# Kernel tuning notes

Hardware: AMD Instinct MI355X
Metric: run time of the kernel (lower is better)

The kernel has to match this reference:

```python
import jax, jax.numpy as jnp
import numpy as np

EPS = 1e-5  # PyTorch BatchNorm3d default eps

def _bn(x, gamma, beta, mean, var):
    # eval-mode batchnorm over channel dim (axis=1) of [B,C,D,H,W]
    inv = jax.lax.rsqrt(var + EPS)
    scale = (gamma * inv)[None, :, None, None, None]
    shift = (beta - mean * gamma * inv)[None, :, None, None, None]
    return x * scale + shift

def _pconv(x, w):
    # 1x1x1 conv3d == channel contraction: w [O,C], x [B,C,D,H,W]
    return jnp.einsum('oc,bcdhw->bodhw', w, x)

def setup_inputs() -> dict:
    key = jax.random.key(0)
    ks = jax.random.split(key, 12)
    B, G, D, H, W = 4, 8, 48, 128, 160
    x1 = jax.random.normal(ks[0], (B, G, D, H, W), dtype=jnp.float32)
    # conv0: G->16 (no bias), BN params for 16 channels
    w0 = jax.random.normal(ks[1], (16, G), dtype=jnp.float32) * 0.1
    g0 = jnp.ones((16,), jnp.float32)
    b0 = jnp.zeros((16,), jnp.float32)
    m0 = jax.random.normal(ks[2], (16,), dtype=jnp.float32) * 0.01
    v0 = jax.random.uniform(ks[3], (16,), jnp.float32, 0.5, 1.5)
    # conv1: 16->8 (no bias), BN params for 8 channels
    w1 = jax.random.normal(ks[4], (8, 16), dtype=jnp.float32) * 0.1
    g1 = jnp.ones((8,), jnp.float32)
    b1 = jnp.zeros((8,), jnp.float32)
    m1 = jax.random.normal(ks[5], (8,), dtype=jnp.float32) * 0.01
    v1 = jax.random.uniform(ks[6], (8,), jnp.float32, 0.5, 1.5)
    # conv2: 8->1 with bias (xavier init)
    lim = float(np.sqrt(6.0 / (8 + 1)))
    w2 = jax.random.uniform(ks[7], (1, 8), jnp.float32, -lim, lim)
    b2 = jnp.zeros((1,), jnp.float32)
    return {"x1": x1, "w0": w0, "g0": g0, "b0": b0, "m0": m0, "v0": v0,
            "w1": w1, "g1": g1, "b1": b1, "m1": m1, "v1": v1,
            "w2": w2, "b2": b2}

def reference(x1, w0, g0, b0, m0, v0, w1, g1, b1, m1, v1, w2, b2):
    h = jax.nn.relu(_bn(_pconv(x1, w0), g0, b0, m0, v0))   # [B,16,D,H,W]
    h = jax.nn.relu(_bn(_pconv(h, w1), g1, b1, m1, v1))    # [B,8,D,H,W]
    h = _pconv(h, w2) + b2[None, :, None, None, None]      # [B,1,D,H,W]
    h = jnp.squeeze(h, axis=1)                             # view -> [B,D,H,W]
    out = jnp.max(jax.nn.sigmoid(h), axis=1)               # max over depth
    return out[:, None]                                    # [B,1,H,W]
```

## Files before the change

### kernel.cpp

```cpp
#include <hip/hip_runtime.h>

#define BATCH 4
#define CIN   8
#define DEPTH 48
#define HGT   128
#define WID   160

#define HW    (HGT*WID)
#define DHW   (DEPTH*HW)
#define CDHW  (CIN*DHW)
#define NPIX  (BATCH*HW)

#define DSPLIT 8
#define DCHUNK (DEPTH/DSPLIT)
#define TILES_PER_B (HW/128)
#define NTILES (NPIX/128)

#define WS_W0P 0
#define WS_S0F 64
#define WS_W1P 80
#define WS_S1F 144
#define WS_W2F 152
#define WS_B2F 160
#define WS_FLAG 384
#define WS_PART 512

typedef _Float16 half2_t __attribute__((ext_vector_type(2)));

static __device__ __forceinline__ float asf(unsigned int u) {
    return __builtin_bit_cast(float, u);
}
static __device__ __forceinline__ unsigned int asu(float f) {
    return __builtin_bit_cast(unsigned int, f);
}
static __device__ __forceinline__ unsigned int pkrtz_u(float a, float b) {
    return __builtin_bit_cast(unsigned int, __builtin_amdgcn_cvt_pkrtz(a, b));
}
static __device__ __forceinline__ float fdot2_u(unsigned int a, unsigned int b, float c) {
    return __builtin_amdgcn_fdot2(__builtin_bit_cast(half2_t, a),
                                  __builtin_bit_cast(half2_t, b), c, false);
}
static __device__ __forceinline__ float ldp(const void* p, int i, bool bf) {
    if (bf) {
        unsigned int u = ((const unsigned short*)p)[i];
        return asf(u << 16);
    }
    return ((const float*)p)[i];
}

__global__ void prep_kernel(const unsigned int* __restrict__ x,
                            const void* __restrict__ w0, const void* __restrict__ g0,
                            const void* __restrict__ b0, const void* __restrict__ m0,
                            const void* __restrict__ v0, const void* __restrict__ w1,
                            const void* __restrict__ g1, const void* __restrict__ b1,
                            const void* __restrict__ m1, const void* __restrict__ v1,
                            const void* __restrict__ w2, const void* __restrict__ b2,
                            float* __restrict__ ws)
{
    unsigned int* wsu = (unsigned int*)ws;
    int t = threadIdx.x;

    int cnt = 0;
    #pragma unroll
    for (int i = 0; i < 16; ++i) {
        unsigned int v = x[(unsigned)(t * 997 + i * 61440 + 12345)];
        if ((((v >> 8) & 0x78u)) == 0x38u) ++cnt;
    }
    #pragma unroll
    for (int off = 32; off > 0; off >>= 1) cnt += __shfl_down(cnt, off, 64);
    cnt = __shfl(cnt, 0, 64);
    bool bf = (cnt >= 512);
    if (t == 0) wsu[WS_FLAG] = bf ? 1u : 0u;

    if (t < 16) {
        float sc = ldp(g0, t, bf) * rsqrtf(ldp(v0, t, bf) + 1e-5f);
        for (int c = 0; c < 4; ++c)
            wsu[WS_W0P + t*4 + c] = pkrtz_u(ldp(w0, t*8 + 2*c, bf) * sc,
                                            ldp(w0, t*8 + 2*c + 1, bf) * sc);
        ws[WS_S0F + t] = ldp(b0, t, bf) - ldp(m0, t, bf) * sc;
    }
    if (t < 8) {
        float sc = ldp(g1, t, bf) * rsqrtf(ldp(v1, t, bf) + 1e-5f);
        for (int c = 0; c < 8; ++c)
            wsu[WS_W1P + t*8 + c] = pkrtz_u(ldp(w1, t*16 + 2*c, bf) * sc,
                                            ldp(w1, t*16 + 2*c + 1, bf) * sc);
        ws[WS_S1F + t] = ldp(b1, t, bf) - ldp(m1, t, bf) * sc;
        ws[WS_W2F + t] = ldp(w2, t, bf);
    }
    if (t == 0) ws[WS_B2F] = ldp(b2, 0, bf);
}

__global__ __launch_bounds__(64, 2) void main_kernel(const void* __restrict__ xv,
                                                     const float* __restrict__ ws,
                                                     float* __restrict__ part)
{
    const unsigned int* wsu = (const unsigned int*)ws;
    bool bf = (wsu[WS_FLAG] != 0u);
    const unsigned int* xb = (const unsigned int*)xv;
    const float2*      xf = (const float2*)xv;

    int lane = threadIdx.x;
    int bid  = blockIdx.x;
    int tile = bid % NTILES;
    int dc   = bid / NTILES;
    int b    = tile / TILES_PER_B;
    int hwp  = (tile % TILES_PER_B) * 64 + lane;
    unsigned bbase = (unsigned)(b * (CDHW/2)) + (unsigned)hwp;
    int d0 = dc * DCHUNK;

    unsigned int W0p[64], W1p[64];
    float S0[16], S1[8], W2[8];
    {
        const uint4* q0 = (const uint4*)(wsu + WS_W0P);
        #pragma unroll
        for (int i = 0; i < 16; ++i) { uint4 q = q0[i]; W0p[4*i]=q.x; W0p[4*i+1]=q.y; W0p[4*i+2]=q.z; W0p[4*i+3]=q.w; }
        const uint4* q1 = (const uint4*)(wsu + WS_W1P);
        #pragma unroll
        for (int i = 0; i < 16; ++i) { uint4 q = q1[i]; W1p[4*i]=q.x; W1p[4*i+1]=q.y; W1p[4*i+2]=q.z; W1p[4*i+3]=q.w; }
        const float4* qs = (const float4*)(ws + WS_S0F);
        #pragma unroll
        for (int i = 0; i < 4; ++i) { float4 f = qs[i]; S0[4*i]=f.x; S0[4*i+1]=f.y; S0[4*i+2]=f.z; S0[4*i+3]=f.w; }
        const float4* qt = (const float4*)(ws + WS_S1F);
        #pragma unroll
        for (int i = 0; i < 2; ++i) { float4 f = qt[i]; S1[4*i]=f.x; S1[4*i+1]=f.y; S1[4*i+2]=f.z; S1[4*i+3]=f.w; }
        const float4* qw = (const float4*)(ws + WS_W2F);
        #pragma unroll
        for (int i = 0; i < 2; ++i) { float4 f = qw[i]; W2[4*i]=f.x; W2[4*i+1]=f.y; W2[4*i+2]=f.z; W2[4*i+3]=f.w; }
    }
    float B2v = ws[WS_B2F];

    float mA = -1e30f, mB = -1e30f;

    #pragma unroll 2
    for (int dd = 0; dd < DCHUNK; ++dd) {
        int d = d0 + dd;
        unsigned idx0 = bbase + (unsigned)(d * (HW/2));

        unsigned int xA[4], xB[4];
        if (bf) {
            unsigned int xd[8];
            #pragma unroll
            for (int c = 0; c < 8; ++c) xd[c] = xb[idx0 + (unsigned)(c * (DHW/2))];
            #pragma unroll
            for (int j = 0; j < 4; ++j) {
                xA[j] = pkrtz_u(asf(xd[2*j] << 16),        asf(xd[2*j+1] << 16));
                xB[j] = pkrtz_u(asf(xd[2*j] & 0xFFFF0000u), asf(xd[2*j+1] & 0xFFFF0000u));
            }
        } else {
            float2 v[8];
            #pragma unroll
            for (int c = 0; c < 8; ++c) v[c] = xf[idx0 + (unsigned)(c * (DHW/2))];
            #pragma unroll
            for (int j = 0; j < 4; ++j) {
                xA[j] = pkrtz_u(v[2*j].x, v[2*j+1].x);
                xB[j] = pkrtz_u(v[2*j].y, v[2*j+1].y);
            }
        }

        float h0A[16], h0B[16];
        #pragma unroll
        for (int o = 0; o < 16; ++o) {
            float a = S0[o], c = S0[o];
            #pragma unroll
            for (int j = 0; j < 4; ++j) {
                a = fdot2_u(xA[j], W0p[o*4 + j], a);
                c = fdot2_u(xB[j], W0p[o*4 + j], c);
            }
            h0A[o] = fmaxf(a, 0.f);
            h0B[o] = fmaxf(c, 0.f);
        }
        unsigned int gA[8], gB[8];
        #pragma unroll
        for (int k = 0; k < 8; ++k) {
            gA[k] = pkrtz_u(h0A[2*k], h0A[2*k+1]);
            gB[k] = pkrtz_u(h0B[2*k], h0B[2*k+1]);
        }

        float sA = B2v, sB = B2v;
        #pragma unroll
        for (int o = 0; o < 8; ++o) {
            float a = S1[o], c = S1[o];
            #pragma unroll
            for (int k = 0; k < 8; ++k) {
                a = fdot2_u(gA[k], W1p[o*8 + k], a);
                c = fdot2_u(gB[k], W1p[o*8 + k], c);
            }
            sA = fmaf(W2[o], fmaxf(a, 0.f), sA);
            sB = fmaf(W2[o], fmaxf(c, 0.f), sB);
        }
        mA = fmaxf(mA, sA);
        mB = fmaxf(mB, sB);
    }

    float2 r; r.x = mA; r.y = mB;
    float2* pp = (float2*)(part + (size_t)dc * NPIX + (size_t)b * HW);
    pp[hwp] = r;
}

__global__ __launch_bounds__(256) void reduce_kernel(const float* __restrict__ part,
                                                     const float* __restrict__ ws,
                                                     void* __restrict__ out)
{
    bool bf = (((const unsigned int*)ws)[WS_FLAG] != 0u);
    int px = blockIdx.x * 256 + threadIdx.x;
    float m = part[px];
    #pragma unroll
    for (int k = 1; k < DSPLIT; ++k) m = fmaxf(m, part[(size_t)k * NPIX + px]);
    float sg = 1.0f / (1.0f + __expf(-m));
    if (bf) {
        unsigned int u = asu(sg);
        unsigned int r = (u + 0x7FFFu + ((u >> 16) & 1u)) >> 16;
        ((unsigned short*)out)[px] = (unsigned short)r;
    } else {
        ((float*)out)[px] = sg;
    }
}

extern "C" void kernel_launch(void* const* d_in, const int* in_sizes, int n_in,
                              void* d_out, int out_size, void* d_ws, size_t ws_size,
                              hipStream_t stream)
{
    float* ws = (float*)d_ws;

    prep_kernel<<<1, 64, 0, stream>>>(
        (const unsigned int*)d_in[0],
        d_in[1], d_in[2], d_in[3], d_in[4], d_in[5], d_in[6],
        d_in[7], d_in[8], d_in[9], d_in[10], d_in[11], d_in[12], ws);

    main_kernel<<<NTILES * DSPLIT, 64, 0, stream>>>(d_in[0], ws, ws + WS_PART);

    reduce_kernel<<<NPIX / 256, 256, 0, stream>>>(ws + WS_PART, ws, d_out);
}
```

Measured before the change: 219.5 us.

## Fuse depth-split reduction into main kernel via shared memory across 8 waves

Each block now has 8 waves, one per depth chunk of the same pixel tile. The per-wave maxima are combined through shared memory and the sigmoid output is written directly, which removes the partial-result buffer and the separate reduce kernel launch. In exchange it adds a block barrier and forces 512-thread blocks, and with the large per-thread register arrays a launch bound of (512,2) may cause register spilling.

```diff
diff --git a/kernel.cpp b/kernel.cpp
--- a/kernel.cpp
+++ b/kernel.cpp
@@ -14,7 +14,7 @@
 #define DSPLIT 8
 #define DCHUNK (DEPTH/DSPLIT)
 #define TILES_PER_B (HW/128)
-#define NTILES (NPIX/128)
+#define NBLK (NPIX/128)
 
 #define WS_W0P 0
 #define WS_S0F 64
@@ -23,7 +23,6 @@
 #define WS_W2F 152
 #define WS_B2F 160
 #define WS_FLAG 384
-#define WS_PART 512
 
 typedef _Float16 half2_t __attribute__((ext_vector_type(2)));
 
@@ -90,23 +89,26 @@
     if (t == 0) ws[WS_B2F] = ldp(b2, 0, bf);
 }
 
-__global__ __launch_bounds__(64, 2) void main_kernel(const void* __restrict__ xv,
-                                                     const float* __restrict__ ws,
-                                                     float* __restrict__ part)
+__global__ __launch_bounds__(512, 2) void main_kernel(const void* __restrict__ xv,
+                                                      const float* __restrict__ ws,
+                                                      void* __restrict__ out)
 {
+    __shared__ float2 sm[DSPLIT][64];
+
     const unsigned int* wsu = (const unsigned int*)ws;
     bool bf = (wsu[WS_FLAG] != 0u);
     const unsigned int* xb = (const unsigned int*)xv;
     const float2*      xf = (const float2*)xv;
 
-    int lane = threadIdx.x;
-    int bid  = blockIdx.x;
-    int tile = bid % NTILES;
-    int dc   = bid / NTILES;
-    int b    = tile / TILES_PER_B;
-    int hwp  = (tile % TILES_PER_B) * 64 + lane;
+    const int tid  = threadIdx.x;
+    const int wave = tid >> 6;
+    const int lane = tid & 63;
+    const int tile = blockIdx.x;
+    const int b    = tile / TILES_PER_B;
+    const int tp   = tile % TILES_PER_B;
+    const int hwp  = tp * 64 + lane;
     unsigned bbase = (unsigned)(b * (CDHW/2)) + (unsigned)hwp;
-    int d0 = dc * DCHUNK;
+    const int d0 = wave * DCHUNK;
 
     unsigned int W0p[64], W1p[64];
     float S0[16], S1[8], W2[8];
@@ -193,26 +195,29 @@
     }
 
     float2 r; r.x = mA; r.y = mB;
-    float2* pp = (float2*)(part + (size_t)dc * NPIX + (size_t)b * HW);
-    pp[hwp] = r;
-}
-
-__global__ __launch_bounds__(256) void reduce_kernel(const float* __restrict__ part,
-                                                     const float* __restrict__ ws,
-                                                     void* __restrict__ out)
-{
-    bool bf = (((const unsigned int*)ws)[WS_FLAG] != 0u);
-    int px = blockIdx.x * 256 + threadIdx.x;
-    float m = part[px];
-    #pragma unroll
-    for (int k = 1; k < DSPLIT; ++k) m = fmaxf(m, part[(size_t)k * NPIX + px]);
-    float sg = 1.0f / (1.0f + __expf(-m));
-    if (bf) {
-        unsigned int u = asu(sg);
-        unsigned int r = (u + 0x7FFFu + ((u >> 16) & 1u)) >> 16;
-        ((unsigned short*)out)[px] = (unsigned short)r;
-    } else {
-        ((float*)out)[px] = sg;
+    sm[wave][lane] = r;
+    __syncthreads();
+
+    if (wave == 0) {
+        float a = -1e30f, c = -1e30f;
+        #pragma unroll
+        for (int k = 0; k < DSPLIT; ++k) {
+            float2 v = sm[k][lane];
+            a = fmaxf(a, v.x);
+            c = fmaxf(c, v.y);
+        }
+        float sa = 1.0f / (1.0f + __expf(-a));
+        float sc = 1.0f / (1.0f + __expf(-c));
+        unsigned outIdx = (unsigned)(b * (HW/2)) + (unsigned)hwp;
+        if (bf) {
+            unsigned int ua = asu(sa), uc = asu(sc);
+            unsigned int ra = (ua + 0x7FFFu + ((ua >> 16) & 1u)) >> 16;
+            unsigned int rc = (uc + 0x7FFFu + ((uc >> 16) & 1u)) >> 16;
+            ((unsigned int*)out)[outIdx] = ra | (rc << 16);
+        } else {
+            float2 o; o.x = sa; o.y = sc;
+            ((float2*)out)[outIdx] = o;
+        }
     }
 }
 
@@ -227,7 +232,5 @@
         d_in[1], d_in[2], d_in[3], d_in[4], d_in[5], d_in[6],
         d_in[7], d_in[8], d_in[9], d_in[10], d_in[11], d_in[12], ws);
 
-    main_kernel<<<NTILES * DSPLIT, 64, 0, stream>>>(d_in[0], ws, ws + WS_PART);
-
-    reduce_kernel<<<NPIX / 256, 256, 0, stream>>>(ws + WS_PART, ws, d_out);
-}
+    main_kernel<<<NBLK, 512, 0, stream>>>(d_in[0], ws, d_out);
+}
```

New measurement: 223.8 us. No clear change (+1.9%).
